# Kernel tuning notes

Hardware: AMD Instinct MI355X
Metric: run time of the kernel (lower is better)

Reference implementation:

```python
import jax, jax.numpy as jnp
import numpy as np

B, S = 2, 1024
NH, NKV, HD = 32, 8, 128
Q_DIM, KV_DIM = NH * HD, NKV * HD
LEVEL = 256
ROPE_BASE = 10000.0


def fq_sym(x, level=LEVEL):
    # symmetric per-tensor fake quant with straight-through estimator
    qp = level // 2 - 1
    s = jnp.maximum(jax.lax.stop_gradient(jnp.max(jnp.abs(x))) / qp, 1e-8)
    q = jnp.clip(jnp.round(x / s), -qp, qp) * s
    return x + jax.lax.stop_gradient(q - x)


def fq_asym(x, level=LEVEL):
    # asymmetric (unsigned) fake quant for values in [0, 1]
    qp = level - 1
    s = jnp.maximum(jax.lax.stop_gradient(jnp.max(x)) / qp, 1e-8)
    q = jnp.clip(jnp.round(x / s), 0, qp) * s
    return x + jax.lax.stop_gradient(q - x)


def rope_tables(seq_len, dim):
    inv_freq = 1.0 / (ROPE_BASE ** (jnp.arange(0, dim, 2, dtype=jnp.float32) / dim))
    freqs = jnp.arange(seq_len, dtype=jnp.float32)[:, None] * inv_freq[None, :]  # [S, HD/2]
    emb = jnp.concatenate([freqs, freqs], axis=-1)  # [S, HD]
    return jnp.cos(emb), jnp.sin(emb)


def rotate_half(x):
    x1, x2 = jnp.split(x, 2, axis=-1)
    return jnp.concatenate([-x2, x1], axis=-1)


def setup_inputs() -> dict:
    key = jax.random.key(0)
    k1, k2, k3, k4 = jax.random.split(key, 4)
    d = Q_DIM + 2 * KV_DIM
    x = jax.random.normal(k1, (B, S, d), dtype=jnp.float32)
    w_qkv = jax.random.normal(k2, (d, d), dtype=jnp.float32) * (d ** -0.5)
    w_o = jax.random.normal(k3, (Q_DIM, Q_DIM), dtype=jnp.float32) * (Q_DIM ** -0.5)
    core_slope = jnp.float32(0.25)
    causal_mask = jnp.where(
        jnp.triu(jnp.ones((S, S), dtype=bool), k=1), jnp.float32(-1e9), jnp.float32(0.0)
    )[None, None]
    return {"x": x, "w_qkv": w_qkv, "w_o": w_o, "core_slope": core_slope,
            "causal_mask": causal_mask}


def reference(x, w_qkv, w_o, core_slope, causal_mask):
    qkv = jnp.einsum("bsd,ed->bse", x, w_qkv)  # Linear, no bias
    q = qkv[..., :Q_DIM].reshape(B, S, NH, HD).transpose(0, 2, 1, 3)
    k = qkv[..., Q_DIM:Q_DIM + KV_DIM].reshape(B, S, NKV, HD).transpose(0, 2, 1, 3)
    v = qkv[..., Q_DIM + KV_DIM:].reshape(B, S, NKV, HD).transpose(0, 2, 1, 3)
    q, k, v = fq_sym(q), fq_sym(k), fq_sym(v)
    cos, sin = rope_tables(S, HD)
    cos, sin = cos[None, None], sin[None, None]  # [1,1,S,HD]
    q = q * cos + rotate_half(q) * sin
    k = k * cos + rotate_half(k) * sin
    groups = NH // NKV
    if groups > 1:
        k = jnp.repeat(k, groups, axis=1)  # [B,NH,S,HD]
        v = jnp.repeat(v, groups, axis=1)
    scale = HD ** -0.5
    scores = jnp.einsum("bhqd,bhkd->bhqk", q, k) * scale
    scores = scores + causal_mask
    attn = jnp.clip(0.5 + core_slope * scores, 0.0, 1.0)  # UniAffineCore -> [0,1]
    attn = fq_asym(attn)
    out = jnp.einsum("bhqk,bhkd->bhqd", attn, v)
    out = fq_sym(out)
    out = out.transpose(0, 2, 1, 3).reshape(B, S, Q_DIM)
    out = jnp.einsum("bsd,ed->bse", out, w_o)
    return fq_sym(out)
```

## Files before the change

kernel.cpp:

```cpp
#include <hip/hip_runtime.h>
#include <stdint.h>

#define BB   2
#define SS   1024
#define NH   32
#define NKV  8
#define HD   128
#define DQ   4096
#define DKV  1024
#define DD   6144
#define MM   2048
#define SCALE 0.08838834764831845f

typedef __attribute__((ext_vector_type(8))) short short8;
typedef __attribute__((ext_vector_type(4))) float f4;

__device__ __forceinline__ float b2f(unsigned short b) {
    union { unsigned int u; float f; } v; v.u = ((unsigned int)b) << 16; return v.f;
}
__device__ __forceinline__ unsigned short f2b(float f) {
    union { float f; unsigned int u; } v; v.f = f;
    unsigned int u = v.u;
    unsigned int r = u + 0x7fffu + ((u >> 16) & 1u);
    return (unsigned short)(r >> 16);
}
__device__ __forceinline__ float fqs(float x, float s) {
    return fminf(fmaxf(rintf(x / s), -127.f), 127.f) * s;
}

typedef const unsigned int __attribute__((address_space(1)))* gas_ptr;
typedef unsigned int __attribute__((address_space(3)))* las_ptr;
__device__ __forceinline__ void gl_lds16(const void* g, void* l) {
    __builtin_amdgcn_global_load_lds((gas_ptr)(uintptr_t)g,
                                     (las_ptr)(unsigned int)(uintptr_t)l, 16, 0, 0);
}

__global__ void detect_kernel(const unsigned short* __restrict__ x, float* scal) {
    __shared__ float w[4];
    int tid = threadIdx.x;
    float m = 0.f;
    for (int i = tid; i < 65536; i += 256) m = fmaxf(m, fabsf(b2f(x[i])));
#pragma unroll
    for (int off = 32; off > 0; off >>= 1) m = fmaxf(m, __shfl_down(m, off));
    if ((tid & 63) == 0) w[tid >> 6] = m;
    __syncthreads();
    if (tid == 0) {
        float mm = fmaxf(fmaxf(w[0], w[1]), fmaxf(w[2], w[3]));
        scal[6] = (mm > 1e4f) ? 1.0f : 0.0f;
    }
}

__global__ void slope_kernel(const unsigned short* __restrict__ sp, float* scal) {
    if (threadIdx.x == 0)
        scal[7] = (scal[6] > 0.5f) ? ((const float*)sp)[0] : b2f(sp[0]);
}

__global__ void convert_split_kernel(const unsigned short* __restrict__ src,
                                     unsigned short* __restrict__ hi,
                                     unsigned short* __restrict__ lo,
                                     const float* __restrict__ scal) {
    size_t t = (size_t)blockIdx.x * 256 + threadIdx.x;
    float v[8] __attribute__((aligned(16)));
    if (scal[6] > 0.5f) {
        const float* s = (const float*)src + t * 8;
        *(float4*)(v)     = *(const float4*)(s);
        *(float4*)(v + 4) = *(const float4*)(s + 4);
    } else {
        unsigned short u[8] __attribute__((aligned(16)));
        *(uint4*)u = *(const uint4*)(src + t * 8);
#pragma unroll
        for (int i = 0; i < 8; i++) v[i] = b2f(u[i]);
    }
    unsigned short h8[8] __attribute__((aligned(16)));
    unsigned short l8[8] __attribute__((aligned(16)));
#pragma unroll
    for (int i = 0; i < 8; i++) {
        unsigned short h = f2b(v[i]);
        h8[i] = h;
        l8[i] = f2b(v[i] - b2f(h));
    }
    *(uint4*)(hi + t * 8) = *(uint4*)h8;
    *(uint4*)(lo + t * 8) = *(uint4*)l8;
}

template<int NT, int MODE>
__global__ __launch_bounds__(256, 2)
void gemm_hilo_kernel(const unsigned short* __restrict__ Ah,
                      const unsigned short* __restrict__ Al,
                      const unsigned short* __restrict__ Bh,
                      const unsigned short* __restrict__ Bl,
                      float* __restrict__ C,
                      int M, int N, int K,
                      float* __restrict__ scal)
{
    __shared__ unsigned short lAh[128 * 32];
    __shared__ unsigned short lAl[(NT == 3) ? 128 * 32 : 8];
    __shared__ unsigned short lBh[128 * 32];
    __shared__ unsigned short lBl[128 * 32];
    __shared__ float wred[4];
    const int tid = threadIdx.x;
    const int bn = blockIdx.x << 7;
    const int bm = blockIdx.y << 7;
    const int wave = tid >> 6, lane = tid & 63;
    const int wm = (wave >> 1) << 6, wn = (wave & 1) << 6;
    const int lm = lane & 15, quad = lane >> 4;

    const f4 z = {0.f, 0.f, 0.f, 0.f};
    f4 acc[4][4];
#pragma unroll
    for (int i = 0; i < 4; i++)
#pragma unroll
        for (int j = 0; j < 4; j++) acc[i][j] = z;

    const int i0 = tid, i1 = tid + 256;
    const size_t ra0 = (size_t)(bm + (i0 >> 2)) * K + (i0 & 3) * 8;
    const size_t ra1 = (size_t)(bm + (i1 >> 2)) * K + (i1 & 3) * 8;
    const size_t rb0 = (size_t)(bn + (i0 >> 2)) * K + (i0 & 3) * 8;
    const size_t rb1 = (size_t)(bn + (i1 >> 2)) * K + (i1 & 3) * 8;

    for (int k0 = 0; k0 < K; k0 += 32) {
        gl_lds16(Ah + ra0 + k0, lAh + i0 * 8);
        gl_lds16(Ah + ra1 + k0, lAh + i1 * 8);
        if (NT == 3) {
            gl_lds16(Al + ra0 + k0, lAl + i0 * 8);
            gl_lds16(Al + ra1 + k0, lAl + i1 * 8);
        }
        gl_lds16(Bh + rb0 + k0, lBh + i0 * 8);
        gl_lds16(Bh + rb1 + k0, lBh + i1 * 8);
        gl_lds16(Bl + rb0 + k0, lBl + i0 * 8);
        gl_lds16(Bl + rb1 + k0, lBl + i1 * 8);
        __syncthreads();
        short8 ah[4], al[4], bh[4], bl[4];
#pragma unroll
        for (int t = 0; t < 4; t++) {
            int ro = (wm + t * 16 + lm) * 32 + quad * 8;
            ah[t] = *(const short8*)(lAh + ro);
            if (NT == 3) al[t] = *(const short8*)(lAl + ro);
        }
#pragma unroll
        for (int t = 0; t < 4; t++) {
            int ro = (wn + t * 16 + lm) * 32 + quad * 8;
            bh[t] = *(const short8*)(lBh + ro);
            bl[t] = *(const short8*)(lBl + ro);
        }
#pragma unroll
        for (int i = 0; i < 4; i++)
#pragma unroll
            for (int j = 0; j < 4; j++) {
                acc[i][j] = __builtin_amdgcn_mfma_f32_16x16x32_bf16(ah[i], bh[j], acc[i][j], 0, 0, 0);
                if (NT == 3)
                    acc[i][j] = __builtin_amdgcn_mfma_f32_16x16x32_bf16(al[i], bh[j], acc[i][j], 0, 0, 0);
                acc[i][j] = __builtin_amdgcn_mfma_f32_16x16x32_bf16(ah[i], bl[j], acc[i][j], 0, 0, 0);
            }
        __syncthreads();
    }

    float mult = 1.f;
    if (MODE == 1) mult = fmaxf(scal[4] / 127.f, 1e-8f);
    float amax = 0.f;
#pragma unroll
    for (int i = 0; i < 4; i++)
#pragma unroll
        for (int j = 0; j < 4; j++)
#pragma unroll
            for (int r = 0; r < 4; r++) {
                float v = acc[i][j][r] * mult;
                amax = fmaxf(amax, fabsf(v));
                size_t row = (size_t)(bm + wm + i * 16 + quad * 4 + r);
                size_t col = (size_t)(bn + wn + j * 16 + lm);
                C[row * (size_t)N + col] = v;
            }
#pragma unroll
    for (int off = 32; off > 0; off >>= 1) amax = fmaxf(amax, __shfl_down(amax, off));
    if (lane == 0) wred[wave] = amax;
    __syncthreads();
    if (tid == 0) {
        float m = fmaxf(fmaxf(wred[0], wred[1]), fmaxf(wred[2], wred[3]));
        int slot = (MODE == 0) ? ((bn < 4096) ? 0 : ((bn < 5120) ? 1 : 2)) : 5;
        atomicMax((unsigned int*)(scal + slot), __float_as_uint(m));
    }
}

__global__ void quant_rope_hilo_kernel(const float* __restrict__ qkv,
                                       unsigned short* __restrict__ Qh,
                                       unsigned short* __restrict__ Ql,
                                       unsigned short* __restrict__ Kh,
                                       unsigned short* __restrict__ Kl,
                                       unsigned short* __restrict__ Vc,
                                       const float* __restrict__ scal)
{
    int t = blockIdx.x * 256 + threadIdx.x;
    int f = t * 8;
    int r = f / DD;
    int c = f - r * DD;
    int b = r >> 10, sp = r & 1023;
    const float* src = qkv + (size_t)r * DD + c;
    float x[8] __attribute__((aligned(16)));
    *(float4*)(x)     = *(const float4*)(src);
    *(float4*)(x + 4) = *(const float4*)(src + 4);

    if (c < 5120) {
        float s; int d; unsigned short *dh, *dl;
        if (c < 4096) {
            s = fmaxf(scal[0] / 127.f, 1e-8f);
            int head = c >> 7; d = c & 127;
            size_t off = (((size_t)(b * NH + head) * SS + sp) << 7) + d;
            dh = Qh + off; dl = Ql + off;
        } else {
            int cc = c - 4096;
            s = fmaxf(scal[1] / 127.f, 1e-8f);
            int head = cc >> 7; d = cc & 127;
            size_t off = (((size_t)(b * NKV + head) * SS + sp) << 7) + d;
            dh = Kh + off; dl = Kl + off;
        }
        int cp = (d < 64) ? (c + 64) : (c - 64);
        float sgn = (d < 64) ? -1.f : 1.f;
        const float* psrc = qkv + (size_t)r * DD + cp;
        float p[8] __attribute__((aligned(16)));
        *(float4*)(p)     = *(const float4*)(psrc);
        *(float4*)(p + 4) = *(const float4*)(psrc + 4);
        unsigned short h8[8] __attribute__((aligned(16)));
        unsigned short l8[8] __attribute__((aligned(16)));
#pragma unroll
        for (int i = 0; i < 8; i++) {
            float xq = fqs(x[i], s);
            float pq = fqs(p[i], s);
            int fi = (d + i) & 63;
            float inv = expf((float)fi * -0.14391156831212787f);
            float ang = (float)sp * inv;
            float sn, cs;
            sincosf(ang, &sn, &cs);
            float o = xq * cs + sgn * pq * sn;
            unsigned short hb = f2b(o);
            h8[i] = hb;
            l8[i] = f2b(o - b2f(hb));
        }
        *(uint4*)(dh) = *(uint4*)h8;
        *(uint4*)(dl) = *(uint4*)l8;
    } else {
        int cc = c - 5120;
        float s = fmaxf(scal[2] / 127.f, 1e-8f);
        int head = cc >> 7, d = cc & 127;
        unsigned short* dst = Vc + (((size_t)(b * NKV + head) * SS + sp) << 7) + d;
        unsigned short o8[8] __attribute__((aligned(16)));
#pragma unroll
        for (int i = 0; i < 8; i++) {
            float code = fminf(fmaxf(rintf(x[i] / s), -127.f), 127.f);
            o8[i] = f2b(code);
        }
        *(uint4*)(dst) = *(uint4*)o8;
    }
}

__global__ void vtrans_kernel(const unsigned short* __restrict__ Vc,
                              unsigned short* __restrict__ Vt)
{
    __shared__ __attribute__((aligned(16))) unsigned short L[64][72];
    const int dtile = blockIdx.x;
    const int ktile = blockIdx.y;
    const int bh    = blockIdx.z;
    const int tid = threadIdx.x;
#pragma unroll
    for (int it = 0; it < 2; it++) {
        int lin = it * 256 + tid;
        int row = lin >> 3, c8 = (lin & 7) * 8;
        *(uint4*)&L[row][c8] =
            *(const uint4*)(Vc + ((size_t)bh * SS + ktile * 64 + row) * HD + dtile * 64 + c8);
    }
    __syncthreads();
#pragma unroll
    for (int it = 0; it < 2; it++) {
        int lin = it * 256 + tid;
        int dr = lin >> 3, k8 = (lin & 7) * 8;
        unsigned short o8[8] __attribute__((aligned(16)));
#pragma unroll
        for (int i = 0; i < 8; i++) o8[i] = L[k8 + i][dr];
        *(uint4*)(Vt + ((size_t)bh * HD + dtile * 64 + dr) * SS + ktile * 64 + k8) = *(uint4*)o8;
    }
}

template<int PASS>
__global__ __launch_bounds__(256, 2)
void attn_mfma_kernel(const unsigned short* __restrict__ Qh,
                      const unsigned short* __restrict__ Ql,
                      const unsigned short* __restrict__ Kh,
                      const unsigned short* __restrict__ Kl,
                      const unsigned short* __restrict__ Vt,
                      float* __restrict__ O,
                      float* __restrict__ scal)
{
    __shared__ __attribute__((aligned(16))) unsigned short Ps[PASS ? 4 : 1][16][72];
    __shared__ float wred[4];
    const int x = blockIdx.x;
    const int qc = x & 15, h = (x >> 4) & 31, b = x >> 9;
    const int hk = h >> 2;
    const int tid = threadIdx.x;
    const int wave = tid >> 6, lane = tid & 63;
    const int lm = lane & 15, quad = lane >> 4;
    const float coef = scal[7] * SCALE;
    float s_a = 1.f, s_av = 1.f;
    if (PASS) {
        s_a = fmaxf(scal[3] / 255.f, 1e-8f);
        float s_v = fmaxf(scal[2] / 127.f, 1e-8f);
        s_av = s_a * s_v;
    }

    const size_t qbase = ((size_t)((b * NH + h) * SS) + qc * 64 + wave * 16 + lm) * HD + quad * 8;
    short8 qh[4], ql[4];
#pragma unroll
    for (int kk = 0; kk < 4; kk++) {
        qh[kk] = *(const short8*)(Qh + qbase + kk * 32);
        ql[kk] = *(const short8*)(Ql + qbase + kk * 32);
    }
    const size_t kbase = (size_t)((b * NKV + hk) * SS) * HD + quad * 8;
    const size_t vbase = (size_t)((b * NKV + hk) * HD) * SS + quad * 8;

    const f4 z = {0.f, 0.f, 0.f, 0.f};
    f4 oacc[8];
    if (PASS) {
#pragma unroll
        for (int j2 = 0; j2 < 8; j2++) oacc[j2] = z;
    }
    float amax = 0.f;
    const int qg = qc * 64 + wave * 16 + quad * 4;

    for (int kt = 0; kt <= qc; kt++) {
        f4 acc[4];
#pragma unroll
        for (int j = 0; j < 4; j++) acc[j] = z;
#pragma unroll
        for (int j = 0; j < 4; j++) {
            const size_t kb = kbase + (size_t)(kt * 64 + j * 16 + lm) * HD;
#pragma unroll
            for (int kk = 0; kk < 4; kk++) {
                short8 kh8 = *(const short8*)(Kh + kb + kk * 32);
                short8 kl8 = *(const short8*)(Kl + kb + kk * 32);
                acc[j] = __builtin_amdgcn_mfma_f32_16x16x32_bf16(qh[kk], kh8, acc[j], 0, 0, 0);
                acc[j] = __builtin_amdgcn_mfma_f32_16x16x32_bf16(ql[kk], kh8, acc[j], 0, 0, 0);
                acc[j] = __builtin_amdgcn_mfma_f32_16x16x32_bf16(qh[kk], kl8, acc[j], 0, 0, 0);
            }
        }
        const bool diag = (kt == qc);
#pragma unroll
        for (int j = 0; j < 4; j++) {
            int kg = kt * 64 + j * 16 + lm;
#pragma unroll
            for (int r = 0; r < 4; r++) {
                bool ok = (!diag) || (kg <= qg + r);
                float a = 0.5f + coef * acc[j][r];
                a = fminf(fmaxf(a, 0.f), 1.f);
                if (PASS == 0) {
                    if (ok) amax = fmaxf(amax, a);
                } else {
                    float cd = ok ? fminf(rintf(a / s_a), 255.f) : 0.f;
                    Ps[wave][quad * 4 + r][j * 16 + lm] = f2b(cd);
                }
            }
        }
        if (PASS) {
            short8 pa0 = *(const short8*)&Ps[wave][lm][quad * 8];
            short8 pa1 = *(const short8*)&Ps[wave][lm][32 + quad * 8];
#pragma unroll
            for (int j2 = 0; j2 < 8; j2++) {
                const unsigned short* vp = Vt + vbase + (size_t)(j2 * 16 + lm) * SS + kt * 64;
                short8 v0 = *(const short8*)(vp);
                short8 v1 = *(const short8*)(vp + 32);
                oacc[j2] = __builtin_amdgcn_mfma_f32_16x16x32_bf16(pa0, v0, oacc[j2], 0, 0, 0);
                oacc[j2] = __builtin_amdgcn_mfma_f32_16x16x32_bf16(pa1, v1, oacc[j2], 0, 0, 0);
            }
        }
    }

    if (PASS == 0) {
#pragma unroll
        for (int off = 32; off > 0; off >>= 1) amax = fmaxf(amax, __shfl_down(amax, off));
        if (lane == 0) wred[wave] = amax;
        __syncthreads();
        if (tid == 0) {
            float m = fmaxf(fmaxf(wred[0], wred[1]), fmaxf(wred[2], wred[3]));
            atomicMax((unsigned int*)(scal + 3), __float_as_uint(m));
        }
    } else {
        float am = 0.f;
        const size_t orow = (size_t)(b * SS + qc * 64 + wave * 16 + quad * 4);
#pragma unroll
        for (int j2 = 0; j2 < 8; j2++)
#pragma unroll
            for (int r = 0; r < 4; r++) {
                float v = oacc[j2][r] * s_av;
                am = fmaxf(am, fabsf(v));
                O[(orow + r) * DQ + h * HD + j2 * 16 + lm] = v;
            }
#pragma unroll
        for (int off = 32; off > 0; off >>= 1) am = fmaxf(am, __shfl_down(am, off));
        if (lane == 0) wred[wave] = am;
        __syncthreads();
        if (tid == 0) {
            float m = fmaxf(fmaxf(wred[0], wred[1]), fmaxf(wred[2], wred[3]));
            atomicMax((unsigned int*)(scal + 4), __float_as_uint(m));
        }
    }
}

__global__ void quant_o_codes_kernel(const float* __restrict__ O,
                                     const float* __restrict__ scal,
                                     unsigned short* __restrict__ Oq)
{
    size_t t = (size_t)blockIdx.x * 256 + threadIdx.x;
    float s = fmaxf(scal[4] / 127.f, 1e-8f);
    float4 v = *(const float4*)(O + t * 4);
    unsigned short o[4] __attribute__((aligned(8)));
    o[0] = f2b(fminf(fmaxf(rintf(v.x / s), -127.f), 127.f));
    o[1] = f2b(fminf(fmaxf(rintf(v.y / s), -127.f), 127.f));
    o[2] = f2b(fminf(fmaxf(rintf(v.z / s), -127.f), 127.f));
    o[3] = f2b(fminf(fmaxf(rintf(v.w / s), -127.f), 127.f));
    *(uint2*)(Oq + t * 4) = *(uint2*)o;
}

__global__ void final_q_kernel(const float* __restrict__ X,
                               const float* __restrict__ scal,
                               float* __restrict__ out)
{
    size_t t = (size_t)blockIdx.x * 256 + threadIdx.x;
    float s = fmaxf(scal[5] / 127.f, 1e-8f);
    float4 v = *(const float4*)(X + t * 4);
    float4 o;
    o.x = fqs(v.x, s);
    o.y = fqs(v.y, s);
    o.z = fqs(v.z, s);
    o.w = fqs(v.w, s);
    *(float4*)(out + t * 4) = o;
}

extern "C" void kernel_launch(void* const* d_in, const int* in_sizes, int n_in,
                              void* d_out, int out_size, void* d_ws, size_t ws_size,
                              hipStream_t stream)
{
    const unsigned short* x      = (const unsigned short*)d_in[0];
    const unsigned short* w_qkv  = (const unsigned short*)d_in[1];
    const unsigned short* w_o    = (const unsigned short*)d_in[2];
    const unsigned short* slope  = (const unsigned short*)d_in[3];
    (void)in_sizes; (void)n_in; (void)out_size; (void)ws_size;

    char* ws = (char*)d_ws;
    float* scal          = (float*)ws;
    unsigned short* xh   = (unsigned short*)(ws + 256);
    unsigned short* xl   = (unsigned short*)(ws + 25166080);
    unsigned short* wqh  = (unsigned short*)(ws + 50331904);
    unsigned short* wql  = (unsigned short*)(ws + 125829376);
    float* qkv           = (float*)(ws + 201326848);
    unsigned short* Qh   = (unsigned short*)(ws + 251658496);
    unsigned short* Ql   = (unsigned short*)(ws + 268435712);
    unsigned short* Kh   = (unsigned short*)(ws + 285212928);
    unsigned short* Kl   = (unsigned short*)(ws + 289407232);
    unsigned short* Vt   = (unsigned short*)(ws + 293601536);
    unsigned short* Vc   = (unsigned short*)(ws + 297795840);
    unsigned short* woh  = (unsigned short*)(ws + 256);
    unsigned short* wol  = (unsigned short*)(ws + 33554688);
    float* O             = (float*)(ws + 67109376);
    unsigned short* Oqc  = (unsigned short*)(ws + 100663808);
    float* out2          = (float*)(ws + 201326848);
    float* outp          = (float*)d_out;

    hipMemsetAsync(scal, 0, 256, stream);
    detect_kernel<<<1, 256, 0, stream>>>(x, scal);
    slope_kernel<<<1, 64, 0, stream>>>(slope, scal);
    convert_split_kernel<<<6144, 256, 0, stream>>>(x, xh, xl, scal);
    convert_split_kernel<<<18432, 256, 0, stream>>>(w_qkv, wqh, wql, scal);
    gemm_hilo_kernel<3, 0><<<dim3(48, 16), 256, 0, stream>>>(xh, xl, wqh, wql, qkv,
                                                             MM, DD, DD, scal);
    quant_rope_hilo_kernel<<<6144, 256, 0, stream>>>(qkv, Qh, Ql, Kh, Kl, Vc, scal);
    vtrans_kernel<<<dim3(2, 16, 16), 256, 0, stream>>>(Vc, Vt);
    convert_split_kernel<<<8192, 256, 0, stream>>>(w_o, woh, wol, scal);
    attn_mfma_kernel<0><<<1024, 256, 0, stream>>>(Qh, Ql, Kh, Kl, Vt, O, scal);
    attn_mfma_kernel<1><<<1024, 256, 0, stream>>>(Qh, Ql, Kh, Kl, Vt, O, scal);
    quant_o_codes_kernel<<<8192, 256, 0, stream>>>(O, scal, Oqc);
    gemm_hilo_kernel<2, 1><<<dim3(32, 16), 256, 0, stream>>>(Oqc, Oqc, woh, wol, out2,
                                                             MM, DQ, DQ, scal);
    final_q_kernel<<<8192, 256, 0, stream>>>(out2, scal, outp);
}
```

Measured before the change: 1.628 ms.

## Double-buffer hi/lo GEMM with swizzled LDS, 2-wave tiles, XCD remap, MFMA priority

The hi/lo split-bf16 GEMM is restructured to use two waves per 128x128 tile, each wave owning a 128x64 sub-tile. LDS becomes double-buffered, with explicit vmcnt waits and raw barriers so global-to-LDS loads for tile t+2 overlap compute on tile t. An XOR swizzle on LDS columns is added to reduce bank conflicts, and block IDs are remapped across groups of 8 (likely XCD-aware) to improve L2 locality. The attention kernel also raises wave priority around its MFMA sections. The cost is more registers per wave (32 accumulators) and fewer waves per CU, and the hand-tuned vmcnt counts are fragile.

```diff
diff --git a/kernel.cpp b/kernel.cpp
--- a/kernel.cpp
+++ b/kernel.cpp
@@ -84,7 +84,7 @@
 }
 
 template<int NT, int MODE>
-__global__ __launch_bounds__(256, 2)
+__global__ __launch_bounds__(128, 1)
 void gemm_hilo_kernel(const unsigned short* __restrict__ Ah,
                       const unsigned short* __restrict__ Al,
                       const unsigned short* __restrict__ Bh,
@@ -93,81 +93,116 @@
                       int M, int N, int K,
                       float* __restrict__ scal)
 {
-    __shared__ unsigned short lAh[128 * 32];
-    __shared__ unsigned short lAl[(NT == 3) ? 128 * 32 : 8];
-    __shared__ unsigned short lBh[128 * 32];
-    __shared__ unsigned short lBl[128 * 32];
-    __shared__ float wred[4];
+    constexpr int PA    = 128 * 32;
+    constexpr int OAL   = PA;
+    constexpr int OBH   = (NT == 3) ? 2 * PA : PA;
+    constexpr int OBL   = OBH + PA;
+    constexpr int BUFSH = OBL + PA;
+    __shared__ unsigned short lds[2 * BUFSH];
+    __shared__ float wred[2];
+
     const int tid = threadIdx.x;
-    const int bn = blockIdx.x << 7;
-    const int bm = blockIdx.y << 7;
     const int wave = tid >> 6, lane = tid & 63;
-    const int wm = (wave >> 1) << 6, wn = (wave & 1) << 6;
     const int lm = lane & 15, quad = lane >> 4;
+    const int qx = quad ^ ((lm >> 1) & 3);
+    const int fo = lm * 32 + qx * 8;
+
+    const int nbn = N >> 7;
+    const int nwg = (M >> 7) * nbn;
+    const int bid = blockIdx.x;
+    const int wg  = (bid & 7) * (nwg >> 3) + (bid >> 3);
+    const int bm  = (wg / nbn) << 7;
+    const int bn  = (wg % nbn) << 7;
+
+    const int rowB = tid >> 2;
+    const int colO = ((tid & 3) ^ ((tid >> 3) & 3)) * 8;
+    const size_t gA = (size_t)bm * K;
+    const size_t gB = (size_t)bn * K;
 
     const f4 z = {0.f, 0.f, 0.f, 0.f};
-    f4 acc[4][4];
-#pragma unroll
-    for (int i = 0; i < 4; i++)
+    f4 acc[8][4];
+#pragma unroll
+    for (int i = 0; i < 8; i++)
 #pragma unroll
         for (int j = 0; j < 4; j++) acc[i][j] = z;
 
-    const int i0 = tid, i1 = tid + 256;
-    const size_t ra0 = (size_t)(bm + (i0 >> 2)) * K + (i0 & 3) * 8;
-    const size_t ra1 = (size_t)(bm + (i1 >> 2)) * K + (i1 & 3) * 8;
-    const size_t rb0 = (size_t)(bn + (i0 >> 2)) * K + (i0 & 3) * 8;
-    const size_t rb1 = (size_t)(bn + (i1 >> 2)) * K + (i1 & 3) * 8;
-
-    for (int k0 = 0; k0 < K; k0 += 32) {
-        gl_lds16(Ah + ra0 + k0, lAh + i0 * 8);
-        gl_lds16(Ah + ra1 + k0, lAh + i1 * 8);
-        if (NT == 3) {
-            gl_lds16(Al + ra0 + k0, lAl + i0 * 8);
-            gl_lds16(Al + ra1 + k0, lAl + i1 * 8);
-        }
-        gl_lds16(Bh + rb0 + k0, lBh + i0 * 8);
-        gl_lds16(Bh + rb1 + k0, lBh + i1 * 8);
-        gl_lds16(Bl + rb0 + k0, lBl + i0 * 8);
-        gl_lds16(Bl + rb1 + k0, lBl + i1 * 8);
-        __syncthreads();
-        short8 ah[4], al[4], bh[4], bl[4];
-#pragma unroll
-        for (int t = 0; t < 4; t++) {
-            int ro = (wm + t * 16 + lm) * 32 + quad * 8;
-            ah[t] = *(const short8*)(lAh + ro);
-            if (NT == 3) al[t] = *(const short8*)(lAl + ro);
-        }
-#pragma unroll
-        for (int t = 0; t < 4; t++) {
-            int ro = (wn + t * 16 + lm) * 32 + quad * 8;
-            bh[t] = *(const short8*)(lBh + ro);
-            bl[t] = *(const short8*)(lBl + ro);
-        }
-#pragma unroll
-        for (int i = 0; i < 4; i++)
+    auto stage = [&](int bsel, int k0) {
+        unsigned short* L = lds + bsel * BUFSH;
+#pragma unroll
+        for (int kk2 = 0; kk2 < 4; kk2++) {
+            int rr = kk2 * 32 + rowB;
+            size_t go = (size_t)rr * K + k0 + colO;
+            int ld = (kk2 * 128 + tid) * 8;
+            gl_lds16(Ah + gA + go, L + ld);
+            if (NT == 3) gl_lds16(Al + gA + go, L + OAL + ld);
+            gl_lds16(Bh + gB + go, L + OBH + ld);
+            gl_lds16(Bl + gB + go, L + OBL + ld);
+        }
+    };
+
+    auto compute = [&](int bsel) {
+        const unsigned short* L = lds + bsel * BUFSH;
+        short8 a_h[8], b_h[4], b_l[4];
+        short8 a_l[(NT == 3) ? 8 : 1];
+#pragma unroll
+        for (int i = 0; i < 8; i++) {
+            a_h[i] = *(const short8*)(L + i * 512 + fo);
+            if (NT == 3) a_l[i] = *(const short8*)(L + OAL + i * 512 + fo);
+        }
+        const int wb = wave * 2048;
+#pragma unroll
+        for (int j = 0; j < 4; j++) {
+            b_h[j] = *(const short8*)(L + OBH + wb + j * 512 + fo);
+            b_l[j] = *(const short8*)(L + OBL + wb + j * 512 + fo);
+        }
+#pragma unroll
+        for (int i = 0; i < 8; i++)
 #pragma unroll
             for (int j = 0; j < 4; j++) {
-                acc[i][j] = __builtin_amdgcn_mfma_f32_16x16x32_bf16(ah[i], bh[j], acc[i][j], 0, 0, 0);
+                acc[i][j] = __builtin_amdgcn_mfma_f32_16x16x32_bf16(a_h[i], b_h[j], acc[i][j], 0, 0, 0);
                 if (NT == 3)
-                    acc[i][j] = __builtin_amdgcn_mfma_f32_16x16x32_bf16(al[i], bh[j], acc[i][j], 0, 0, 0);
-                acc[i][j] = __builtin_amdgcn_mfma_f32_16x16x32_bf16(ah[i], bl[j], acc[i][j], 0, 0, 0);
+                    acc[i][j] = __builtin_amdgcn_mfma_f32_16x16x32_bf16(a_l[i], b_h[j], acc[i][j], 0, 0, 0);
+                acc[i][j] = __builtin_amdgcn_mfma_f32_16x16x32_bf16(a_h[i], b_l[j], acc[i][j], 0, 0, 0);
             }
-        __syncthreads();
-    }
+    };
+
+#define WAITV do { if (NT == 3) asm volatile("s_waitcnt vmcnt(16)" ::: "memory"); \
+                   else         asm volatile("s_waitcnt vmcnt(12)" ::: "memory"); } while (0)
+#define WAIT0 asm volatile("s_waitcnt vmcnt(0)" ::: "memory")
+#define SCHED0 __builtin_amdgcn_sched_barrier(0)
+#define RBAR  __builtin_amdgcn_s_barrier()
+
+    const int nt = K >> 5;
+    stage(0, 0);
+    stage(1, 32);
+    for (int t = 0; t + 2 < nt; ++t) {
+        WAITV;
+        RBAR; SCHED0;
+        compute(t & 1);
+        SCHED0; RBAR; SCHED0;
+        stage(t & 1, (t + 2) << 5);
+    }
+    WAITV;  RBAR; SCHED0; compute(nt & 1);
+    WAIT0;  RBAR; SCHED0; compute((nt - 1) & 1);
+
+#undef WAITV
+#undef WAIT0
+#undef SCHED0
+#undef RBAR
 
     float mult = 1.f;
     if (MODE == 1) mult = fmaxf(scal[4] / 127.f, 1e-8f);
     float amax = 0.f;
 #pragma unroll
-    for (int i = 0; i < 4; i++)
+    for (int i = 0; i < 8; i++)
 #pragma unroll
         for (int j = 0; j < 4; j++)
 #pragma unroll
             for (int r = 0; r < 4; r++) {
                 float v = acc[i][j][r] * mult;
                 amax = fmaxf(amax, fabsf(v));
-                size_t row = (size_t)(bm + wm + i * 16 + quad * 4 + r);
-                size_t col = (size_t)(bn + wn + j * 16 + lm);
+                size_t row = (size_t)(bm + i * 16 + quad * 4 + r);
+                size_t col = (size_t)(bn + wave * 64 + j * 16 + lm);
                 C[row * (size_t)N + col] = v;
             }
 #pragma unroll
@@ -175,7 +210,7 @@
     if (lane == 0) wred[wave] = amax;
     __syncthreads();
     if (tid == 0) {
-        float m = fmaxf(fmaxf(wred[0], wred[1]), fmaxf(wred[2], wred[3]));
+        float m = fmaxf(wred[0], wred[1]);
         int slot = (MODE == 0) ? ((bn < 4096) ? 0 : ((bn < 5120) ? 1 : 2)) : 5;
         atomicMax((unsigned int*)(scal + slot), __float_as_uint(m));
     }
@@ -328,6 +363,7 @@
         f4 acc[4];
 #pragma unroll
         for (int j = 0; j < 4; j++) acc[j] = z;
+        __builtin_amdgcn_s_setprio(1);
 #pragma unroll
         for (int j = 0; j < 4; j++) {
             const size_t kb = kbase + (size_t)(kt * 64 + j * 16 + lm) * HD;
@@ -340,6 +376,7 @@
                 acc[j] = __builtin_amdgcn_mfma_f32_16x16x32_bf16(qh[kk], kl8, acc[j], 0, 0, 0);
             }
         }
+        __builtin_amdgcn_s_setprio(0);
         const bool diag = (kt == qc);
 #pragma unroll
         for (int j = 0; j < 4; j++) {
@@ -360,6 +397,7 @@
         if (PASS) {
             short8 pa0 = *(const short8*)&Ps[wave][lm][quad * 8];
             short8 pa1 = *(const short8*)&Ps[wave][lm][32 + quad * 8];
+            __builtin_amdgcn_s_setprio(1);
 #pragma unroll
             for (int j2 = 0; j2 < 8; j2++) {
                 const unsigned short* vp = Vt + vbase + (size_t)(j2 * 16 + lm) * SS + kt * 64;
@@ -368,6 +406,7 @@
                 oacc[j2] = __builtin_amdgcn_mfma_f32_16x16x32_bf16(pa0, v0, oacc[j2], 0, 0, 0);
                 oacc[j2] = __builtin_amdgcn_mfma_f32_16x16x32_bf16(pa1, v1, oacc[j2], 0, 0, 0);
             }
+            __builtin_amdgcn_s_setprio(0);
         }
     }
 
@@ -467,15 +506,15 @@
     slope_kernel<<<1, 64, 0, stream>>>(slope, scal);
     convert_split_kernel<<<6144, 256, 0, stream>>>(x, xh, xl, scal);
     convert_split_kernel<<<18432, 256, 0, stream>>>(w_qkv, wqh, wql, scal);
-    gemm_hilo_kernel<3, 0><<<dim3(48, 16), 256, 0, stream>>>(xh, xl, wqh, wql, qkv,
-                                                             MM, DD, DD, scal);
+    gemm_hilo_kernel<3, 0><<<768, 128, 0, stream>>>(xh, xl, wqh, wql, qkv,
+                                                    MM, DD, DD, scal);
     quant_rope_hilo_kernel<<<6144, 256, 0, stream>>>(qkv, Qh, Ql, Kh, Kl, Vc, scal);
     vtrans_kernel<<<dim3(2, 16, 16), 256, 0, stream>>>(Vc, Vt);
     convert_split_kernel<<<8192, 256, 0, stream>>>(w_o, woh, wol, scal);
     attn_mfma_kernel<0><<<1024, 256, 0, stream>>>(Qh, Ql, Kh, Kl, Vt, O, scal);
     attn_mfma_kernel<1><<<1024, 256, 0, stream>>>(Qh, Ql, Kh, Kl, Vt, O, scal);
     quant_o_codes_kernel<<<8192, 256, 0, stream>>>(O, scal, Oqc);
-    gemm_hilo_kernel<2, 1><<<dim3(32, 16), 256, 0, stream>>>(Oqc, Oqc, woh, wol, out2,
-                                                             MM, DQ, DQ, scal);
+    gemm_hilo_kernel<2, 1><<<512, 128, 0, stream>>>(Oqc, Oqc, woh, wol, out2,
+                                                    MM, DQ, DQ, scal);
     final_q_kernel<<<8192, 256, 0, stream>>>(out2, scal, outp);
 }
```

Measured after the change: 1.860 ms. 1.14x slower.
